# Kernel optimization log

Measured on AMD Instinct MI355X. Metric: run time of the kernel, lower is better.

## Reference

```python
import jax, jax.numpy as jnp
import numpy as np

WINDOW = 7
N_HEADS = 4
EMBED = 128
N_TOK = WINDOW * WINDOW  # 49
N_WIN = 64               # windows per image (56x56 feature map / 7)
BATCH_IMG = 64
B = N_WIN * BATCH_IMG    # 4096


def make_rel_index(w):
    ch = np.arange(w)
    coords = np.stack(np.meshgrid(ch, ch), axis=0).reshape(2, -1)  # (2, w*w)
    rel = coords[:, :, None] - coords[:, None, :]                  # (2, N, N)
    rel = rel.transpose(1, 2, 0)
    rel[:, :, 0] += w - 1
    rel[:, :, 1] += w - 1
    rel[:, :, 0] *= 2 * w - 1
    return jnp.asarray(rel.sum(-1), dtype=jnp.int32)               # (N, N)


def setup_inputs() -> dict:
    key = jax.random.key(0)
    ks = jax.random.split(key, 6)
    x = jax.random.normal(ks[0], (B, N_TOK, EMBED), dtype=jnp.float32)
    qkv_w = jax.random.normal(ks[1], (EMBED, 3 * EMBED), dtype=jnp.float32) * (EMBED ** -0.5)
    qkv_b = jnp.zeros((3 * EMBED,), dtype=jnp.float32)
    proj_w = jax.random.normal(ks[2], (EMBED, EMBED), dtype=jnp.float32) * (EMBED ** -0.5)
    proj_b = jnp.zeros((EMBED,), dtype=jnp.float32)
    bias_table = jax.random.normal(ks[3], ((2 * WINDOW - 1) ** 2, N_HEADS), dtype=jnp.float32) * 0.02
    # shift mask: additive, 0 or large negative; use random binary * -100 to mimic Swin shift mask
    mask_bits = jax.random.bernoulli(ks[4], 0.2, (N_WIN, N_TOK, N_TOK))
    mask = jnp.where(mask_bits, jnp.float32(-100.0), jnp.float32(0.0))
    rel_index = make_rel_index(WINDOW)
    return {"x": x, "qkv_w": qkv_w, "qkv_b": qkv_b, "proj_w": proj_w,
            "proj_b": proj_b, "bias_table": bias_table, "mask": mask,
            "rel_index": rel_index}


def reference(x, qkv_w, qkv_b, proj_w, proj_b, bias_table, mask, rel_index):
    Bt, N, C = x.shape
    h = N_HEADS
    d = C // h
    scale = d ** -0.5
    qkv = (x @ qkv_w + qkv_b).reshape(Bt, N, 3, h, d)
    q, k, v = jnp.moveaxis(qkv, 2, 0)                      # each (B, N, h, d)
    q = q * scale
    attn = jnp.einsum('bnhd,bmhd->bhnm', q, k)             # (B, h, N, N)
    bias = bias_table[rel_index.reshape(-1)].reshape(N, N, h)
    attn = attn + jnp.transpose(bias, (2, 0, 1))[None]     # add rel-pos bias
    nW = mask.shape[0]
    attn = attn.reshape(Bt // nW, nW, h, N, N) + mask[None, :, None]
    attn = jax.nn.softmax(attn.reshape(Bt, h, N, N), axis=-1)
    out = jnp.einsum('bhnm,bmhd->bnhd', attn, v).reshape(Bt, N, C)
    return out @ proj_w + proj_b
```

## Files before the change

kernel.cpp:

```cpp
#include <hip/hip_runtime.h>

#define NTOK 49
#define CDIM 128
#define NH 4
#define NWIN 64

typedef unsigned short u16;
typedef __bf16 bf16x8 __attribute__((ext_vector_type(8)));
typedef float f32x4 __attribute__((ext_vector_type(4)));
typedef u16 u16x4 __attribute__((ext_vector_type(4)));

__device__ __forceinline__ u16 f2bf(float f) {
  unsigned int u = __float_as_uint(f);
  u += 0x7fffu + ((u >> 16) & 1u);
  return (u16)(u >> 16);
}

__device__ __forceinline__ bf16x8 ld8(const u16* p) { return *(const bf16x8*)p; }

__global__ void prep_kernel(const float* __restrict__ qkv_w,
                            const float* __restrict__ proj_w,
                            const float* __restrict__ bias_table,
                            const float* __restrict__ mask,
                            const int* __restrict__ rel_index,
                            u16* __restrict__ wqkvT,
                            u16* __restrict__ wprojT,
                            float* __restrict__ cmb) {
  int i = blockIdx.x * 256 + threadIdx.x;
  if (i < 384 * 128) {
    int n = i >> 7, k = i & 127;
    wqkvT[i] = f2bf(qkv_w[k * 384 + n]);
  }
  if (i < 128 * 128) {
    int n = i >> 7, k = i & 127;
    wprojT[i] = f2bf(proj_w[k * 128 + n]);
  }
  int m = i & 63, n2 = (i >> 6) & 63, hh = (i >> 12) & 3, win = i >> 14;
  float v = -1e30f;
  if (n2 < NTOK && m < NTOK)
    v = bias_table[rel_index[n2 * NTOK + m] * NH + hh] + mask[(win * NTOK + n2) * NTOK + m];
  cmb[i] = v;
}

#define HQ(h) (8192 + (h) * 6144)
#define HK(h) (HQ(h) + 2048)
#define HV(h) (HQ(h) + 4096)
#define HP(h) (HQ(h))

__device__ __forceinline__ int xsw(int row, int col) {
  return (row << 7) + ((((col >> 3) ^ (row & 15)) << 3) | (col & 7));
}

__global__ __launch_bounds__(256, 2)
void swin_fused(const float* __restrict__ x, const float* __restrict__ qkv_b,
                const float* __restrict__ proj_b, const u16* __restrict__ wqkvT,
                const u16* __restrict__ wprojT, const float* __restrict__ cmb,
                float* __restrict__ out) {
  __shared__ u16 lds[32768];
  const int tid  = threadIdx.x;
  const int w    = tid >> 6;
  const int lane = tid & 63;
  const int ln   = lane & 15;
  const int quad = lane >> 4;
  const int b    = blockIdx.x;
  const int win  = b & (NWIN - 1);
  const float scale = 0.17677669529663687f;

  {
    const float4* x4 = (const float4*)(x + (size_t)b * (NTOK * CDIM));
    for (int i = tid; i < (NTOK * CDIM) / 4; i += 256) {
      float4 f = x4[i];
      int e = i << 2;
      int row = e >> 7, col = e & 127;
      u16x4 v;
      v[0] = f2bf(f.x); v[1] = f2bf(f.y); v[2] = f2bf(f.z); v[3] = f2bf(f.w);
      *(u16x4*)&lds[xsw(row, col)] = v;
    }
    for (int i = tid; i < (15 * CDIM) / 4; i += 256) {
      int e = i << 2;
      int row = NTOK + (e >> 7), col = e & 127;
      u16x4 v = {0, 0, 0, 0};
      *(u16x4*)&lds[xsw(row, col)] = v;
    }
  }
  __syncthreads();

  for (int tnl = 0; tnl < 6; ++tnl) {
    int tn = w * 6 + tnl;
    int colg = tn * 16 + ln;
    bf16x8 bw[4];
#pragma unroll
    for (int ks = 0; ks < 4; ++ks)
      bw[ks] = ld8(wqkvT + colg * 128 + ks * 32 + quad * 8);
    float cb = qkv_b[colg];
    int sect = colg >> 7;
    int cc = colg & 127;
    int hh = cc >> 5, dd = cc & 31;
#pragma unroll
    for (int tm = 0; tm < 4; ++tm) {
      f32x4 acc = {0.f, 0.f, 0.f, 0.f};
#pragma unroll
      for (int ks = 0; ks < 4; ++ks) {
        bf16x8 af = ld8(&lds[xsw(tm * 16 + ln, ks * 32 + quad * 8)]);
        acc = __builtin_amdgcn_mfma_f32_16x16x32_bf16(af, bw[ks], acc, 0, 0, 0);
      }
      int row0 = tm * 16 + quad * 4;
      if (sect == 0) {
#pragma unroll
        for (int r = 0; r < 4; ++r)
          lds[HQ(hh) + (row0 + r) * 32 + dd] = f2bf((acc[r] + cb) * scale);
      } else if (sect == 1) {
#pragma unroll
        for (int r = 0; r < 4; ++r)
          lds[HK(hh) + (row0 + r) * 32 + dd] = f2bf(acc[r] + cb);
      } else {
        u16x4 v;
#pragma unroll
        for (int r = 0; r < 4; ++r) v[r] = f2bf(acc[r] + cb);
        *(u16x4*)&lds[HV(hh) + dd * 64 + row0] = v;
      }
    }
  }
  __syncthreads();

  f32x4 s[4][4];
  {
    bf16x8 aq[4];
#pragma unroll
    for (int tm = 0; tm < 4; ++tm)
      aq[tm] = ld8(&lds[HQ(w) + (tm * 16 + ln) * 32 + quad * 8]);
#pragma unroll
    for (int tn = 0; tn < 4; ++tn) {
      bf16x8 bk = ld8(&lds[HK(w) + (tn * 16 + ln) * 32 + quad * 8]);
#pragma unroll
      for (int tm = 0; tm < 4; ++tm) {
        f32x4 z = {0.f, 0.f, 0.f, 0.f};
        s[tm][tn] = __builtin_amdgcn_mfma_f32_16x16x32_bf16(aq[tm], bk, z, 0, 0, 0);
      }
    }
  }
  {
    const float* cb = cmb + ((size_t)((win << 2) | w) << 12);
#pragma unroll
    for (int tm = 0; tm < 4; ++tm) {
      int row0 = tm * 16 + quad * 4;
#pragma unroll
      for (int tn = 0; tn < 4; ++tn) {
        int col = tn * 16 + ln;
#pragma unroll
        for (int r = 0; r < 4; ++r)
          s[tm][tn][r] += cb[(row0 + r) * 64 + col];
      }
    }
  }
#pragma unroll
  for (int tm = 0; tm < 4; ++tm) {
    int row0 = tm * 16 + quad * 4;
#pragma unroll
    for (int r = 0; r < 4; ++r) {
      float vm = fmaxf(fmaxf(s[tm][0][r], s[tm][1][r]), fmaxf(s[tm][2][r], s[tm][3][r]));
      vm = fmaxf(vm, __shfl_xor(vm, 1));
      vm = fmaxf(vm, __shfl_xor(vm, 2));
      vm = fmaxf(vm, __shfl_xor(vm, 4));
      vm = fmaxf(vm, __shfl_xor(vm, 8));
      float e[4];
#pragma unroll
      for (int tn = 0; tn < 4; ++tn) e[tn] = __expf(s[tm][tn][r] - vm);
      float sum = e[0] + e[1] + e[2] + e[3];
      sum += __shfl_xor(sum, 1);
      sum += __shfl_xor(sum, 2);
      sum += __shfl_xor(sum, 4);
      sum += __shfl_xor(sum, 8);
      float inv = 1.0f / sum;
      int rr = row0 + r;
#pragma unroll
      for (int tn = 0; tn < 4; ++tn)
        lds[HP(w) + rr * 64 + tn * 16 + ln] = f2bf(e[tn] * inv);
    }
  }

  {
    f32x4 o[4][2];
#pragma unroll
    for (int tm = 0; tm < 4; ++tm)
#pragma unroll
      for (int tn = 0; tn < 2; ++tn) { f32x4 z = {0.f,0.f,0.f,0.f}; o[tm][tn] = z; }
#pragma unroll
    for (int ks = 0; ks < 2; ++ks) {
      bf16x8 pa[4];
#pragma unroll
      for (int tm = 0; tm < 4; ++tm)
        pa[tm] = ld8(&lds[HP(w) + (tm * 16 + ln) * 64 + ks * 32 + quad * 8]);
#pragma unroll
      for (int tn = 0; tn < 2; ++tn) {
        bf16x8 vb = ld8(&lds[HV(w) + (tn * 16 + ln) * 64 + ks * 32 + quad * 8]);
#pragma unroll
        for (int tm = 0; tm < 4; ++tm)
          o[tm][tn] = __builtin_amdgcn_mfma_f32_16x16x32_bf16(pa[tm], vb, o[tm][tn], 0, 0, 0);
      }
    }
#pragma unroll
    for (int tm = 0; tm < 4; ++tm) {
      int row0 = tm * 16 + quad * 4;
#pragma unroll
      for (int tn = 0; tn < 2; ++tn) {
        int c = w * 32 + tn * 16 + ln;
#pragma unroll
        for (int r = 0; r < 4; ++r)
          lds[xsw(row0 + r, c)] = f2bf(o[tm][tn][r]);
      }
    }
  }
  __syncthreads();

  {
    bf16x8 aof[4][4];
#pragma unroll
    for (int tm = 0; tm < 4; ++tm)
#pragma unroll
      for (int ks = 0; ks < 4; ++ks)
        aof[tm][ks] = ld8(&lds[xsw(tm * 16 + ln, ks * 32 + quad * 8)]);
#pragma unroll
    for (int tj = 0; tj < 2; ++tj) {
      int tn = w * 2 + tj;
      int colg = tn * 16 + ln;
      bf16x8 bw[4];
#pragma unroll
      for (int ks = 0; ks < 4; ++ks)
        bw[ks] = ld8(wprojT + colg * 128 + ks * 32 + quad * 8);
      float pb = proj_b[colg];
#pragma unroll
      for (int tm = 0; tm < 4; ++tm) {
        f32x4 acc = {0.f, 0.f, 0.f, 0.f};
#pragma unroll
        for (int ks = 0; ks < 4; ++ks)
          acc = __builtin_amdgcn_mfma_f32_16x16x32_bf16(aof[tm][ks], bw[ks], acc, 0, 0, 0);
        int row0 = tm * 16 + quad * 4;
#pragma unroll
        for (int r = 0; r < 4; ++r) {
          int rr = row0 + r;
          if (rr < NTOK)
            out[((size_t)b * NTOK + rr) * CDIM + colg] = acc[r] + pb;
        }
      }
    }
  }
}

extern "C" void kernel_launch(void* const* d_in, const int* in_sizes, int n_in,
                              void* d_out, int out_size, void* d_ws, size_t ws_size,
                              hipStream_t stream) {
  const float* x          = (const float*)d_in[0];
  const float* qkv_w      = (const float*)d_in[1];
  const float* qkv_b      = (const float*)d_in[2];
  const float* proj_w     = (const float*)d_in[3];
  const float* proj_b     = (const float*)d_in[4];
  const float* bias_table = (const float*)d_in[5];
  const float* mask       = (const float*)d_in[6];
  const int*   rel_index  = (const int*)d_in[7];

  u16*   wqkvT  = (u16*)d_ws;
  u16*   wprojT = wqkvT + 384 * 128;
  float* cmb    = (float*)((char*)d_ws + 131072);

  const int Bt = in_sizes[0] / (NTOK * CDIM);

  prep_kernel<<<4096, 256, 0, stream>>>(qkv_w, proj_w, bias_table, mask, rel_index,
                                        wqkvT, wprojT, cmb);
  swin_fused<<<Bt, 256, 0, stream>>>(x, qkv_b, proj_b, wqkvT, wprojT, cmb, (float*)d_out);
}
```

Before: 326.1 us.

## Restructure per-head LDS layout, keep V in registers, transpose bias table

The QKV projection is reorganized so each wave computes the Q, K and V columns for its own head. This removes the block-wide barrier between the QKV GEMM and attention. V stays in registers as packed bf16 pairs and is redistributed to the PV MFMA operand layout with cross-lane shuffles instead of a transposed LDS store. Q/K/P/O regions use padded row strides, and the bias+mask table is stored transposed so each lane reads it as one float4 vector load. LDS per block shrinks to 52 KB and launch bounds are raised to 3 blocks per CU, at the cost of more shuffles and register pressure.

Measured after the change: 314.2 us. 3.6% less time.

```diff
diff --git a/kernel.cpp b/kernel.cpp
--- a/kernel.cpp
+++ b/kernel.cpp
@@ -6,16 +6,19 @@
 #define NWIN 64
 
 typedef unsigned short u16;
+typedef unsigned int u32;
 typedef __bf16 bf16x8 __attribute__((ext_vector_type(8)));
 typedef float f32x4 __attribute__((ext_vector_type(4)));
 typedef u16 u16x4 __attribute__((ext_vector_type(4)));
 
 __device__ __forceinline__ u16 f2bf(float f) {
-  unsigned int u = __float_as_uint(f);
+  u32 u = __float_as_uint(f);
   u += 0x7fffu + ((u >> 16) & 1u);
   return (u16)(u >> 16);
 }
-
+__device__ __forceinline__ u32 pack2(float a, float b) {
+  return (u32)f2bf(a) | ((u32)f2bf(b) << 16);
+}
 __device__ __forceinline__ bf16x8 ld8(const u16* p) { return *(const bf16x8*)p; }
 
 __global__ void prep_kernel(const float* __restrict__ qkv_w,
@@ -25,7 +28,7 @@
                             const int* __restrict__ rel_index,
                             u16* __restrict__ wqkvT,
                             u16* __restrict__ wprojT,
-                            float* __restrict__ cmb) {
+                            float* __restrict__ cmbT) {
   int i = blockIdx.x * 256 + threadIdx.x;
   if (i < 384 * 128) {
     int n = i >> 7, k = i & 127;
@@ -35,28 +38,25 @@
     int n = i >> 7, k = i & 127;
     wprojT[i] = f2bf(proj_w[k * 128 + n]);
   }
-  int m = i & 63, n2 = (i >> 6) & 63, hh = (i >> 12) & 3, win = i >> 14;
+  int n = i & 63, m = (i >> 6) & 63, hh = (i >> 12) & 3, win = i >> 14;
   float v = -1e30f;
-  if (n2 < NTOK && m < NTOK)
-    v = bias_table[rel_index[n2 * NTOK + m] * NH + hh] + mask[(win * NTOK + n2) * NTOK + m];
-  cmb[i] = v;
-}
-
-#define HQ(h) (8192 + (h) * 6144)
-#define HK(h) (HQ(h) + 2048)
-#define HV(h) (HQ(h) + 4096)
-#define HP(h) (HQ(h))
+  if (n < NTOK && m < NTOK)
+    v = bias_table[rel_index[n * NTOK + m] * NH + hh] + mask[(win * NTOK + n) * NTOK + m];
+  cmbT[i] = v;
+}
+
+#define RGN(h) (8192 + (h) * 4608)
 
 __device__ __forceinline__ int xsw(int row, int col) {
   return (row << 7) + ((((col >> 3) ^ (row & 15)) << 3) | (col & 7));
 }
 
-__global__ __launch_bounds__(256, 2)
+__global__ __launch_bounds__(256, 3)
 void swin_fused(const float* __restrict__ x, const float* __restrict__ qkv_b,
                 const float* __restrict__ proj_b, const u16* __restrict__ wqkvT,
-                const u16* __restrict__ wprojT, const float* __restrict__ cmb,
+                const u16* __restrict__ wprojT, const float* __restrict__ cmbT,
                 float* __restrict__ out) {
-  __shared__ u16 lds[32768];
+  __shared__ u16 lds[26624];
   const int tid  = threadIdx.x;
   const int w    = tid >> 6;
   const int lane = tid & 63;
@@ -85,53 +85,56 @@
   }
   __syncthreads();
 
-  for (int tnl = 0; tnl < 6; ++tnl) {
-    int tn = w * 6 + tnl;
-    int colg = tn * 16 + ln;
-    bf16x8 bw[4];
-#pragma unroll
-    for (int ks = 0; ks < 4; ++ks)
-      bw[ks] = ld8(wqkvT + colg * 128 + ks * 32 + quad * 8);
-    float cb = qkv_b[colg];
-    int sect = colg >> 7;
-    int cc = colg & 127;
-    int hh = cc >> 5, dd = cc & 31;
-#pragma unroll
-    for (int tm = 0; tm < 4; ++tm) {
-      f32x4 acc = {0.f, 0.f, 0.f, 0.f};
-#pragma unroll
-      for (int ks = 0; ks < 4; ++ks) {
-        bf16x8 af = ld8(&lds[xsw(tm * 16 + ln, ks * 32 + quad * 8)]);
-        acc = __builtin_amdgcn_mfma_f32_16x16x32_bf16(af, bw[ks], acc, 0, 0, 0);
-      }
-      int row0 = tm * 16 + quad * 4;
-      if (sect == 0) {
-#pragma unroll
-        for (int r = 0; r < 4; ++r)
-          lds[HQ(hh) + (row0 + r) * 32 + dd] = f2bf((acc[r] + cb) * scale);
-      } else if (sect == 1) {
-#pragma unroll
-        for (int r = 0; r < 4; ++r)
-          lds[HK(hh) + (row0 + r) * 32 + dd] = f2bf(acc[r] + cb);
-      } else {
-        u16x4 v;
-#pragma unroll
-        for (int r = 0; r < 4; ++r) v[r] = f2bf(acc[r] + cb);
-        *(u16x4*)&lds[HV(hh) + dd * 64 + row0] = v;
-      }
-    }
-  }
-  __syncthreads();
+  u32 vbx[4][2], vby[4][2];
+  {
+    bf16x8 af[4][4];
+#pragma unroll
+    for (int tm = 0; tm < 4; ++tm)
+#pragma unroll
+      for (int ks = 0; ks < 4; ++ks)
+        af[tm][ks] = ld8(&lds[xsw(tm * 16 + ln, ks * 32 + quad * 8)]);
+
+#pragma unroll
+    for (int tl = 0; tl < 6; ++tl) {
+      int sect = tl >> 1, tc = tl & 1;
+      int colg = sect * 128 + w * 32 + tc * 16 + ln;
+      bf16x8 bw[4];
+#pragma unroll
+      for (int ks = 0; ks < 4; ++ks)
+        bw[ks] = ld8(wqkvT + colg * 128 + ks * 32 + quad * 8);
+      float cb = qkv_b[colg];
+#pragma unroll
+      for (int tm = 0; tm < 4; ++tm) {
+        f32x4 acc = {0.f, 0.f, 0.f, 0.f};
+#pragma unroll
+        for (int ks = 0; ks < 4; ++ks)
+          acc = __builtin_amdgcn_mfma_f32_16x16x32_bf16(af[tm][ks], bw[ks], acc, 0, 0, 0);
+        int row0 = tm * 16 + quad * 4;
+        if (sect == 0) {
+#pragma unroll
+          for (int r = 0; r < 4; ++r)
+            lds[RGN(w) + (row0 + r) * 36 + tc * 16 + ln] = f2bf((acc[r] + cb) * scale);
+        } else if (sect == 1) {
+#pragma unroll
+          for (int r = 0; r < 4; ++r)
+            lds[RGN(w) + 2304 + (row0 + r) * 36 + tc * 16 + ln] = f2bf(acc[r] + cb);
+        } else {
+          vbx[tm][tc] = pack2(acc[0] + cb, acc[1] + cb);
+          vby[tm][tc] = pack2(acc[2] + cb, acc[3] + cb);
+        }
+      }
+    }
+  }
 
   f32x4 s[4][4];
   {
     bf16x8 aq[4];
 #pragma unroll
     for (int tm = 0; tm < 4; ++tm)
-      aq[tm] = ld8(&lds[HQ(w) + (tm * 16 + ln) * 32 + quad * 8]);
+      aq[tm] = ld8(&lds[RGN(w) + (tm * 16 + ln) * 36 + quad * 8]);
 #pragma unroll
     for (int tn = 0; tn < 4; ++tn) {
-      bf16x8 bk = ld8(&lds[HK(w) + (tn * 16 + ln) * 32 + quad * 8]);
+      bf16x8 bk = ld8(&lds[RGN(w) + 2304 + (tn * 16 + ln) * 36 + quad * 8]);
 #pragma unroll
       for (int tm = 0; tm < 4; ++tm) {
         f32x4 z = {0.f, 0.f, 0.f, 0.f};
@@ -140,16 +143,13 @@
     }
   }
   {
-    const float* cb = cmb + ((size_t)((win << 2) | w) << 12);
+    const float* cb = cmbT + ((size_t)((win << 2) | w) << 12);
 #pragma unroll
     for (int tm = 0; tm < 4; ++tm) {
-      int row0 = tm * 16 + quad * 4;
 #pragma unroll
       for (int tn = 0; tn < 4; ++tn) {
-        int col = tn * 16 + ln;
-#pragma unroll
-        for (int r = 0; r < 4; ++r)
-          s[tm][tn][r] += cb[(row0 + r) * 64 + col];
+        f32x4 c4 = *(const f32x4*)&cb[(tn * 16 + ln) * 64 + tm * 16 + quad * 4];
+        s[tm][tn] += c4;
       }
     }
   }
@@ -175,7 +175,7 @@
       int rr = row0 + r;
 #pragma unroll
       for (int tn = 0; tn < 4; ++tn)
-        lds[HP(w) + rr * 64 + tn * 16 + ln] = f2bf(e[tn] * inv);
+        lds[RGN(w) + rr * 68 + tn * 16 + ln] = f2bf(e[tn] * inv);
     }
   }
 
@@ -184,31 +184,36 @@
 #pragma unroll
     for (int tm = 0; tm < 4; ++tm)
 #pragma unroll
-      for (int tn = 0; tn < 2; ++tn) { f32x4 z = {0.f,0.f,0.f,0.f}; o[tm][tn] = z; }
+      for (int tc = 0; tc < 2; ++tc) { f32x4 z = {0.f,0.f,0.f,0.f}; o[tm][tc] = z; }
 #pragma unroll
     for (int ks = 0; ks < 2; ++ks) {
       bf16x8 pa[4];
 #pragma unroll
       for (int tm = 0; tm < 4; ++tm)
-        pa[tm] = ld8(&lds[HP(w) + (tm * 16 + ln) * 64 + ks * 32 + quad * 8]);
-#pragma unroll
-      for (int tn = 0; tn < 2; ++tn) {
-        bf16x8 vb = ld8(&lds[HV(w) + (tn * 16 + ln) * 64 + ks * 32 + quad * 8]);
+        pa[tm] = ld8(&lds[RGN(w) + (tm * 16 + ln) * 68 + ks * 32 + quad * 8]);
+#pragma unroll
+      for (int tc = 0; tc < 2; ++tc) {
+        union { u32 u[4]; bf16x8 v; } bv;
+#pragma unroll
+        for (int p = 0; p < 4; ++p) {
+          int src = ((2 * (quad & 1) + (p >> 1)) << 4) | ln;
+          int a0 = __shfl((int)((p & 1) ? vby[2 * ks][tc]     : vbx[2 * ks][tc]),     src);
+          int a1 = __shfl((int)((p & 1) ? vby[2 * ks + 1][tc] : vbx[2 * ks + 1][tc]), src);
+          bv.u[p] = (u32)((quad < 2) ? a0 : a1);
+        }
 #pragma unroll
         for (int tm = 0; tm < 4; ++tm)
-          o[tm][tn] = __builtin_amdgcn_mfma_f32_16x16x32_bf16(pa[tm], vb, o[tm][tn], 0, 0, 0);
+          o[tm][tc] = __builtin_amdgcn_mfma_f32_16x16x32_bf16(pa[tm], bv.v, o[tm][tc], 0, 0, 0);
       }
     }
 #pragma unroll
     for (int tm = 0; tm < 4; ++tm) {
       int row0 = tm * 16 + quad * 4;
 #pragma unroll
-      for (int tn = 0; tn < 2; ++tn) {
-        int c = w * 32 + tn * 16 + ln;
+      for (int tc = 0; tc < 2; ++tc)
 #pragma unroll
         for (int r = 0; r < 4; ++r)
-          lds[xsw(row0 + r, c)] = f2bf(o[tm][tn][r]);
-      }
+          lds[RGN(w) + 2304 + (row0 + r) * 36 + tc * 16 + ln] = f2bf(o[tm][tc][r]);
     }
   }
   __syncthreads();
@@ -219,11 +224,10 @@
     for (int tm = 0; tm < 4; ++tm)
 #pragma unroll
       for (int ks = 0; ks < 4; ++ks)
-        aof[tm][ks] = ld8(&lds[xsw(tm * 16 + ln, ks * 32 + quad * 8)]);
+        aof[tm][ks] = ld8(&lds[RGN(ks) + 2304 + (tm * 16 + ln) * 36 + quad * 8]);
 #pragma unroll
     for (int tj = 0; tj < 2; ++tj) {
-      int tn = w * 2 + tj;
-      int colg = tn * 16 + ln;
+      int colg = w * 32 + tj * 16 + ln;
       bf16x8 bw[4];
 #pragma unroll
       for (int ks = 0; ks < 4; ++ks)
@@ -261,11 +265,11 @@
 
   u16*   wqkvT  = (u16*)d_ws;
   u16*   wprojT = wqkvT + 384 * 128;
-  float* cmb    = (float*)((char*)d_ws + 131072);
+  float* cmbT   = (float*)((char*)d_ws + 131072);
 
   const int Bt = in_sizes[0] / (NTOK * CDIM);
 
   prep_kernel<<<4096, 256, 0, stream>>>(qkv_w, proj_w, bias_table, mask, rel_index,
-                                        wqkvT, wprojT, cmb);
-  swin_fused<<<Bt, 256, 0, stream>>>(x, qkv_b, proj_b, wqkvT, wprojT, cmb, (float*)d_out);
-}
+                                        wqkvT, wprojT, cmbT);
+  swin_fused<<<Bt, 256, 0, stream>>>(x, qkv_b, proj_b, wqkvT, wprojT, cmbT, (float*)d_out);
+}
```
